# Kernel optimization log

Measured on AMD Instinct MI355X. Metric: run time of the kernel, lower is better.

Reference implementation:

```python
import jax, jax.numpy as jnp
import numpy as np

B, H, W, T = 2, 48, 48, 48
DIM, NH, KS = 384, 6, 3
HD = DIM // NH
K3 = KS ** 3  # 27 local neighbors


def setup_inputs() -> dict:
    key = jax.random.key(0)
    k1, k2, k3 = jax.random.split(key, 3)
    q = jax.random.normal(k1, (B, H, W, T, DIM), dtype=jnp.float32)
    k = jax.random.normal(k2, (B, H, W, T, DIM), dtype=jnp.float32)
    rpb = jax.random.normal(k3, (NH, KS, KS, KS), dtype=jnp.float32) * 0.02
    # fixed displacement vectors: meshgrid of [-1, 0, 1]^3, 'ij' indexing -> (27, 3)
    vec = jnp.arange(-(KS // 2), KS // 2 + 1, dtype=jnp.float32)
    grid = jnp.stack(jnp.meshgrid(vec, vec, vec, indexing='ij'), axis=-1)
    v = grid.reshape(K3, 3)
    return {"q": q, "k": k, "rpb": rpb, "v": v}


def reference(q, k, rpb, v):
    scale = HD ** (-0.5)
    # (B,H,W,T,NH,HD), pre-scaled queries
    qh = q.reshape(B, H, W, T, NH, HD) * scale
    kh = k.reshape(B, H, W, T, NH, HD)
    pdr = KS // 2
    k_pad = jnp.pad(kh, ((0, 0), (pdr, pdr), (pdr, pdr), (pdr, pdr), (0, 0), (0, 0)))
    # local QK logits: for each of the 27 offsets, dot q with the shifted k.
    # Loop is over a fixed tiny neighborhood (27), not over data dims, and
    # avoids materializing a [27,B,H,W,T,C] gather tensor.
    logits = []
    for di in range(KS):
        for dj in range(KS):
            for dl in range(KS):
                ks = k_pad[:, di:di + H, dj:dj + W, dl:dl + T]  # (B,H,W,T,NH,HD)
                logits.append(jnp.einsum('bxyznd,bxyznd->bxyzn', qh, ks))
    attn = jnp.stack(logits, axis=-1)  # (B,H,W,T,NH,27)
    attn = attn + rpb.reshape(NH, K3)  # relative position bias
    attn = jax.nn.softmax(attn, axis=-1)
    # weighted sum of fixed displacement vectors: (B,H,W,T,NH,3)
    x = jnp.einsum('bxyzno,oc->bxyznc', attn, v)
    x = x.reshape(B, H, W, T, NH * 3)
    return x.transpose(0, 4, 1, 2, 3)  # (B, NH*3, H, W, T)
```

## Files before the change

kernel.cpp:

```cpp
#include <hip/hip_runtime.h>

namespace {

constexpr int HH  = 48;
constexpr int DIM = 384;
constexpr int NH  = 6;
constexpr int K3  = 27;
constexpr float SCALE = 0.125f;

constexpr int TT     = 4;
constexpr int NPAD   = 224;
constexpr int NT     = 7;
constexpr int TILES1 = HH / TT;
constexpr int TILES  = TILES1 * TILES1 * TILES1;
constexpr int NBLK   = 2 * NH * TILES;

typedef _Float16 half8  __attribute__((ext_vector_type(8)));
typedef _Float16 half2v __attribute__((ext_vector_type(2)));
typedef __fp16   fp16x2 __attribute__((ext_vector_type(2)));
typedef float    floatx4 __attribute__((ext_vector_type(4)));

__device__ __forceinline__ half2v pk(float a, float b) {
    fp16x2 t = __builtin_amdgcn_cvt_pkrtz(a, b);
    return __builtin_bit_cast(half2v, t);
}

__global__ __launch_bounds__(256, 4)
void natten_mfma2(const float* __restrict__ q, const float* __restrict__ k,
                  const float* __restrict__ rpb, const float* __restrict__ vv,
                  float* __restrict__ out)
{
    __shared__ _Float16 k_lds[NPAD * 64];
    __shared__ float    logit_lds[64 * 28];
    __shared__ float4   rv_lds[K3];

    const int bid0 = blockIdx.x;
    const int bid  = (bid0 & 7) * (NBLK / 8) + (bid0 >> 3);

    const int n    = bid % NH;
    const int tile = (bid / NH) % TILES;
    const int b    = bid / (NH * TILES);
    const int tz = (tile % TILES1) * TT;
    const int ty = ((tile / TILES1) % TILES1) * TT;
    const int tx = (tile / (TILES1 * TILES1)) * TT;

    const int tid = threadIdx.x;
    char* kl = (char*)k_lds;

    if (tid < K3) {
        rv_lds[tid] = make_float4(vv[tid * 3], vv[tid * 3 + 1], vv[tid * 3 + 2],
                                  rpb[n * K3 + tid]);
    }

    const float* kb = k + (size_t)b * (HH * HH * HH) * DIM + n * 64;
    {
        const int col0 = tid >> 3;
        const int ch   = tid & 7;
        int cx = 0, cy = col0 / 6, cz = col0 - (col0 / 6) * 6;
        const int xm = (col0 & 7) << 4;
        char* dst = kl + col0 * 128 + ((ch * 16) ^ xm);
        #pragma unroll
        for (int it = 0; it < 7; ++it) {
            const int gx = tx + cx - 1, gy = ty + cy - 1, gz = tz + cz - 1;
            float4 f0 = make_float4(0.f, 0.f, 0.f, 0.f), f1 = f0;
            if ((unsigned)gx < 48u && (unsigned)gy < 48u && (unsigned)gz < 48u) {
                const float* s = kb + (size_t)((gx * 48 + gy) * 48 + gz) * DIM + ch * 8;
                f0 = ((const float4*)s)[0];
                f1 = ((const float4*)s)[1];
            }
            half8 h;
            ((half2v*)&h)[0] = pk(f0.x, f0.y);
            ((half2v*)&h)[1] = pk(f0.z, f0.w);
            ((half2v*)&h)[2] = pk(f1.x, f1.y);
            ((half2v*)&h)[3] = pk(f1.z, f1.w);
            *(half8*)(dst + it * 4096) = h;
            cz += 2; if (cz >= 6) { cz -= 6; cy += 1; }
            cy += 5; if (cy >= 6) { cy -= 6; cx += 1; }
        }
    }

    const int w = tid >> 6, lane = tid & 63;
    const int lrow = lane & 15, lgrp = lane >> 4;
    half8 a0, a1;
    {
        const float* qp = q + (size_t)b * (HH * HH * HH) * DIM
            + (size_t)(((tx + w) * 48 + (ty + (lrow >> 2))) * 48 + (tz + (lrow & 3))) * DIM
            + n * 64 + lgrp * 8;
        float4 f0 = ((const float4*)qp)[0];
        float4 f1 = ((const float4*)qp)[1];
        float4 g0 = ((const float4*)(qp + 32))[0];
        float4 g1 = ((const float4*)(qp + 32))[1];
        ((half2v*)&a0)[0] = pk(f0.x, f0.y);
        ((half2v*)&a0)[1] = pk(f0.z, f0.w);
        ((half2v*)&a0)[2] = pk(f1.x, f1.y);
        ((half2v*)&a0)[3] = pk(f1.z, f1.w);
        ((half2v*)&a1)[0] = pk(g0.x, g0.y);
        ((half2v*)&a1)[1] = pk(g0.z, g0.w);
        ((half2v*)&a1)[2] = pk(g1.x, g1.y);
        ((half2v*)&a1)[3] = pk(g1.z, g1.w);
    }
    __syncthreads();

    const int cbase = w * 36 + lrow;
    const int xm2 = (cbase & 7) << 4;
    const char* bpA = kl + cbase * 128 + ((lgrp * 16) ^ xm2);
    const char* bpB = kl + cbase * 128 + ((lgrp * 16 + 64) ^ xm2);
    floatx4 acc[NT];
    #pragma unroll
    for (int nt = 0; nt < NT; ++nt) {
        const half8 b0 = *(const half8*)(bpA + nt * 2048);
        const half8 b1 = *(const half8*)(bpB + nt * 2048);
        floatx4 c = {0.f, 0.f, 0.f, 0.f};
        c = __builtin_amdgcn_mfma_f32_16x16x32_f16(a0, b0, c, 0, 0, 0);
        c = __builtin_amdgcn_mfma_f32_16x16x32_f16(a1, b1, c, 0, 0, 0);
        acc[nt] = c;
    }

    {
        const int ly6 = lrow >= 12 ? 2 : (lrow >= 6 ? 1 : 0);
        const int lz6 = lrow - ly6 * 6;
        const int base0 = (w * 16 + lgrp * 4) * 112;
        constexpr int Nx[NT] = {0, 0, 0, 1, 1, 2, 2};
        constexpr int Ny[NT] = {0, 2, 5, 2, 4, 1, 4};
        constexpr int Nz[NT] = {0, 4, 2, 0, 4, 2, 0};
        #pragma unroll
        for (int nt = 0; nt < NT; ++nt) {
            int rz = lz6 + Nz[nt];
            int ry = ly6 + Ny[nt];
            if (rz >= 6) { rz -= 6; ry += 1; }
            int rx = Nx[nt];
            if (ry >= 6) { ry -= 6; rx += 1; }
            const int dj = ry - lgrp;
            if (rx <= 2 && (unsigned)dj <= 2u) {
                const int sl0 = (rx * 3 + dj) * 3 + rz;
                #pragma unroll
                for (int r = 0; r < 4; ++r) {
                    if ((unsigned)(rz - r) <= 2u) {
                        *(float*)((char*)logit_lds + base0 + r * 112 + (sl0 - r) * 4)
                            = acc[nt][r];
                    }
                }
            }
        }
    }
    __syncthreads();

    {
        const int qi = tid >> 2, p = tid & 3;
        const float* lp = logit_lds + qi * 28;
        float t[7];
        float mx = -1e30f;
        #pragma unroll
        for (int j = 0; j < 7; ++j) {
            const int o = p + 4 * j;
            if (o < K3) {
                t[j] = fmaf(lp[o], SCALE, rv_lds[o].w);
                mx = fmaxf(mx, t[j]);
            }
        }
        mx = fmaxf(mx, __shfl_xor(mx, 1));
        mx = fmaxf(mx, __shfl_xor(mx, 2));
        float den = 0.f, n0 = 0.f, n1 = 0.f, n2 = 0.f;
        #pragma unroll
        for (int j = 0; j < 7; ++j) {
            const int o = p + 4 * j;
            if (o < K3) {
                const float e = __expf(t[j] - mx);
                const float4 rv = rv_lds[o];
                den += e;
                n0 = fmaf(e, rv.x, n0);
                n1 = fmaf(e, rv.y, n1);
                n2 = fmaf(e, rv.z, n2);
            }
        }
        den += __shfl_xor(den, 1); den += __shfl_xor(den, 2);
        n0  += __shfl_xor(n0, 1);  n0  += __shfl_xor(n0, 2);
        n1  += __shfl_xor(n1, 1);  n1  += __shfl_xor(n1, 2);
        n2  += __shfl_xor(n2, 1);  n2  += __shfl_xor(n2, 2);
        if (p < 3) {
            const float res = (p == 0 ? n0 : (p == 1 ? n1 : n2)) / den;
            out[((size_t)(b * 18 + n * 3 + p) * HH + (tx + (qi >> 4))) * (size_t)(HH * HH)
                + (size_t)(ty + ((qi >> 2) & 3)) * HH + (tz + (qi & 3))] = res;
        }
    }
}

}

extern "C" void kernel_launch(void* const* d_in, const int* in_sizes, int n_in,
                              void* d_out, int out_size, void* d_ws, size_t ws_size,
                              hipStream_t stream)
{
    (void)in_sizes; (void)n_in; (void)d_ws; (void)ws_size; (void)out_size;
    const float* q   = (const float*)d_in[0];
    const float* k   = (const float*)d_in[1];
    const float* rpb = (const float*)d_in[2];
    const float* vv  = (const float*)d_in[3];
    float* out = (float*)d_out;

    natten_mfma2<<<dim3(NBLK), dim3(256), 0, stream>>>(q, k, rpb, vv, out);
}
```

Measured before the change: 199.5 us.

## Batch K/Q global loads before conversion, alias logit LDS onto K tile, use exp2

All seven K rows and the Q fragment are loaded unconditionally, with clamped addresses and a zero mask, before any fp16 conversion or LDS store. This puts more loads in flight to hide global latency. The logit buffer now reuses the K tile's shared memory behind an extra barrier, which cuts LDS per block, and launch bounds rise to 5 blocks per CU. Softmax folds log2(e) into the scale and bias and uses the hardware exp2. The cost is more registers held live by the batched loads and redundant loads at boundary tiles.

```diff
diff --git a/kernel.cpp b/kernel.cpp
--- a/kernel.cpp
+++ b/kernel.cpp
@@ -6,7 +6,8 @@
 constexpr int DIM = 384;
 constexpr int NH  = 6;
 constexpr int K3  = 27;
-constexpr float SCALE = 0.125f;
+constexpr float L2E    = 1.44269504088896f;
+constexpr float SCALE2 = 0.125f * L2E;
 
 constexpr int TT     = 4;
 constexpr int NPAD   = 224;
@@ -25,14 +26,14 @@
     return __builtin_bit_cast(half2v, t);
 }
 
-__global__ __launch_bounds__(256, 4)
-void natten_mfma2(const float* __restrict__ q, const float* __restrict__ k,
+__global__ __launch_bounds__(256, 5)
+void natten_mfma3(const float* __restrict__ q, const float* __restrict__ k,
                   const float* __restrict__ rpb, const float* __restrict__ vv,
                   float* __restrict__ out)
 {
     __shared__ _Float16 k_lds[NPAD * 64];
-    __shared__ float    logit_lds[64 * 28];
     __shared__ float4   rv_lds[K3];
+    float* logit_lds = (float*)k_lds;
 
     const int bid0 = blockIdx.x;
     const int bid  = (bid0 & 7) * (NBLK / 8) + (bid0 >> 3);
@@ -49,31 +50,30 @@
 
     if (tid < K3) {
         rv_lds[tid] = make_float4(vv[tid * 3], vv[tid * 3 + 1], vv[tid * 3 + 2],
-                                  rpb[n * K3 + tid]);
+                                  rpb[n * K3 + tid] * L2E);
     }
 
     const float* kb = k + (size_t)b * (HH * HH * HH) * DIM + n * 64;
+    const int col0 = tid >> 3;
+    const int ch   = tid & 7;
+    char* dst = kl + col0 * 128 + ((ch * 16) ^ ((col0 & 7) << 4));
+
+    float4 F0[7], F1[7];
+    float  MS[7];
     {
-        const int col0 = tid >> 3;
-        const int ch   = tid & 7;
         int cx = 0, cy = col0 / 6, cz = col0 - (col0 / 6) * 6;
-        const int xm = (col0 & 7) << 4;
-        char* dst = kl + col0 * 128 + ((ch * 16) ^ xm);
         #pragma unroll
         for (int it = 0; it < 7; ++it) {
             const int gx = tx + cx - 1, gy = ty + cy - 1, gz = tz + cz - 1;
-            float4 f0 = make_float4(0.f, 0.f, 0.f, 0.f), f1 = f0;
-            if ((unsigned)gx < 48u && (unsigned)gy < 48u && (unsigned)gz < 48u) {
-                const float* s = kb + (size_t)((gx * 48 + gy) * 48 + gz) * DIM + ch * 8;
-                f0 = ((const float4*)s)[0];
-                f1 = ((const float4*)s)[1];
-            }
-            half8 h;
-            ((half2v*)&h)[0] = pk(f0.x, f0.y);
-            ((half2v*)&h)[1] = pk(f0.z, f0.w);
-            ((half2v*)&h)[2] = pk(f1.x, f1.y);
-            ((half2v*)&h)[3] = pk(f1.z, f1.w);
-            *(half8*)(dst + it * 4096) = h;
+            const bool valid = ((unsigned)gx < 48u) && ((unsigned)gy < 48u) &&
+                               ((unsigned)gz < 48u);
+            const int cgx = min(max(gx, 0), 47);
+            const int cgy = min(max(gy, 0), 47);
+            const int cgz = min(max(gz, 0), 47);
+            const float* s = kb + (size_t)((cgx * 48 + cgy) * 48 + cgz) * DIM + ch * 8;
+            F0[it] = ((const float4*)s)[0];
+            F1[it] = ((const float4*)s)[1];
+            MS[it] = valid ? 1.f : 0.f;
             cz += 2; if (cz >= 6) { cz -= 6; cy += 1; }
             cy += 5; if (cy >= 6) { cy -= 6; cx += 1; }
         }
@@ -81,24 +81,34 @@
 
     const int w = tid >> 6, lane = tid & 63;
     const int lrow = lane & 15, lgrp = lane >> 4;
+    const float* qp = q + (size_t)b * (HH * HH * HH) * DIM
+        + (size_t)(((tx + w) * 48 + (ty + (lrow >> 2))) * 48 + (tz + (lrow & 3))) * DIM
+        + n * 64 + lgrp * 8;
+    const float4 qf0 = ((const float4*)qp)[0];
+    const float4 qf1 = ((const float4*)qp)[1];
+    const float4 qg0 = ((const float4*)(qp + 32))[0];
+    const float4 qg1 = ((const float4*)(qp + 32))[1];
+
+    #pragma unroll
+    for (int it = 0; it < 7; ++it) {
+        const float m = MS[it];
+        half8 h;
+        ((half2v*)&h)[0] = pk(F0[it].x * m, F0[it].y * m);
+        ((half2v*)&h)[1] = pk(F0[it].z * m, F0[it].w * m);
+        ((half2v*)&h)[2] = pk(F1[it].x * m, F1[it].y * m);
+        ((half2v*)&h)[3] = pk(F1[it].z * m, F1[it].w * m);
+        *(half8*)(dst + it * 4096) = h;
+    }
+
     half8 a0, a1;
-    {
-        const float* qp = q + (size_t)b * (HH * HH * HH) * DIM
-            + (size_t)(((tx + w) * 48 + (ty + (lrow >> 2))) * 48 + (tz + (lrow & 3))) * DIM
-            + n * 64 + lgrp * 8;
-        float4 f0 = ((const float4*)qp)[0];
-        float4 f1 = ((const float4*)qp)[1];
-        float4 g0 = ((const float4*)(qp + 32))[0];
-        float4 g1 = ((const float4*)(qp + 32))[1];
-        ((half2v*)&a0)[0] = pk(f0.x, f0.y);
-        ((half2v*)&a0)[1] = pk(f0.z, f0.w);
-        ((half2v*)&a0)[2] = pk(f1.x, f1.y);
-        ((half2v*)&a0)[3] = pk(f1.z, f1.w);
-        ((half2v*)&a1)[0] = pk(g0.x, g0.y);
-        ((half2v*)&a1)[1] = pk(g0.z, g0.w);
-        ((half2v*)&a1)[2] = pk(g1.x, g1.y);
-        ((half2v*)&a1)[3] = pk(g1.z, g1.w);
-    }
+    ((half2v*)&a0)[0] = pk(qf0.x, qf0.y);
+    ((half2v*)&a0)[1] = pk(qf0.z, qf0.w);
+    ((half2v*)&a0)[2] = pk(qf1.x, qf1.y);
+    ((half2v*)&a0)[3] = pk(qf1.z, qf1.w);
+    ((half2v*)&a1)[0] = pk(qg0.x, qg0.y);
+    ((half2v*)&a1)[1] = pk(qg0.z, qg0.w);
+    ((half2v*)&a1)[2] = pk(qg1.x, qg1.y);
+    ((half2v*)&a1)[3] = pk(qg1.z, qg1.w);
     __syncthreads();
 
     const int cbase = w * 36 + lrow;
@@ -115,6 +125,7 @@
         c = __builtin_amdgcn_mfma_f32_16x16x32_f16(a1, b1, c, 0, 0, 0);
         acc[nt] = c;
     }
+    __syncthreads();
 
     {
         const int ly6 = lrow >= 12 ? 2 : (lrow >= 6 ? 1 : 0);
@@ -154,7 +165,7 @@
         for (int j = 0; j < 7; ++j) {
             const int o = p + 4 * j;
             if (o < K3) {
-                t[j] = fmaf(lp[o], SCALE, rv_lds[o].w);
+                t[j] = fmaf(lp[o], SCALE2, rv_lds[o].w);
                 mx = fmaxf(mx, t[j]);
             }
         }
@@ -165,7 +176,7 @@
         for (int j = 0; j < 7; ++j) {
             const int o = p + 4 * j;
             if (o < K3) {
-                const float e = __expf(t[j] - mx);
+                const float e = __builtin_amdgcn_exp2f(t[j] - mx);
                 const float4 rv = rv_lds[o];
                 den += e;
                 n0 = fmaf(e, rv.x, n0);
@@ -198,5 +209,5 @@
     const float* vv  = (const float*)d_in[3];
     float* out = (float*)d_out;
 
-    natten_mfma2<<<dim3(NBLK), dim3(256), 0, stream>>>(q, k, rpb, vv, out);
-}
+    natten_mfma3<<<dim3(NBLK), dim3(256), 0, stream>>>(q, k, rpb, vv, out);
+}
```

Result: no change. 198.0 us (-0.7%).
